# Kernel optimization log

Hardware: AMD Instinct MI355X
Metric: run time of the kernel (lower is better)

## Reference

```python
import jax, jax.numpy as jnp
import numpy as np

B, CIN, COUT, H, W = 8, 64, 64, 32, 64


def _conv3x3(x, w, b):
    # x: [B,Cin,H,W], w: [Cout,Cin,3,3], b: [Cout]; SAME padding (pad=1)
    y = jax.lax.conv_general_dilated(
        x, w, window_strides=(1, 1), padding=((1, 1), (1, 1)),
        dimension_numbers=('NCHW', 'OIHW', 'NCHW'))
    return y + b[None, :, None, None]


def setup_inputs() -> dict:
    key = jax.random.key(0)
    ks = jax.random.split(key, 7)
    fan_in = CIN * 3 * 3
    s = 1.0 / np.sqrt(fan_in)
    x = jax.random.normal(ks[0], (B, CIN, H, W), dtype=jnp.float32)
    wq = jax.random.uniform(ks[1], (COUT, CIN, 3, 3), jnp.float32, -s, s)
    bq = jax.random.uniform(ks[2], (COUT,), jnp.float32, -s, s)
    wk = jax.random.uniform(ks[3], (COUT, CIN, 3, 3), jnp.float32, -s, s)
    bk = jax.random.uniform(ks[4], (COUT,), jnp.float32, -s, s)
    wv = jax.random.uniform(ks[5], (COUT, CIN, 3, 3), jnp.float32, -s, s)
    bv = jax.random.uniform(ks[6], (COUT,), jnp.float32, -s, s)
    return {"x": x, "wq": wq, "bq": bq, "wk": wk, "bk": bk, "wv": wv, "bv": bv}


def reference(x, wq, bq, wk, bk, wv, bv):
    b, _, h, w = x.shape
    n = h * w
    q = _conv3x3(x, wq, bq).reshape(b, COUT, n)  # [B,C,N]
    k = _conv3x3(x, wk, bk).reshape(b, COUT, n)
    v = _conv3x3(x, wv, bv).reshape(b, COUT, n)
    # scores[b, i, j] = sum_c q[b,c,i] * k[b,c,j]  (NOTE: no 1/sqrt(d) scaling, as in source)
    scores = jnp.einsum('bci,bcj->bij', q, k)      # [B,N,N]
    attn = jax.nn.softmax(scores, axis=-1)
    out = jnp.einsum('bij,bcj->bci', attn, v)      # attn @ V^T, then transpose -> [B,C,N]
    return out.reshape(b, COUT, h, w)
```

## Files before the change

kernel.cpp:

```cpp
#include <hip/hip_runtime.h>
#include <hip/hip_bf16.h>

#define BATCH 8
#define NC    64
#define HH    32
#define WW    64
#define NN    2048
#define NCP   72
#define NCHUNK 4

typedef __attribute__((ext_vector_type(8))) short bf16x8;
typedef __attribute__((ext_vector_type(4))) short short4v;
typedef __attribute__((ext_vector_type(4))) float f32x4;

__device__ __forceinline__ unsigned short f2bf(float f) {
    union { float f; unsigned u; } v; v.f = f;
    unsigned r = v.u + 0x7fffu + ((v.u >> 16) & 1u);
    return (unsigned short)(r >> 16);
}
__device__ __forceinline__ float bf2f(unsigned short h) {
    union { unsigned u; float f; } v; v.u = ((unsigned)h) << 16;
    return v.f;
}

__device__ __forceinline__ bf16x8 load8(const unsigned short* a, const unsigned short* b) {
    short4v lo = *(const short4v*)a;
    short4v hi = *(const short4v*)b;
    return __builtin_shufflevector(lo, hi, 0, 1, 2, 3, 4, 5, 6, 7);
}

__device__ __forceinline__ int ci_of_slot(int j) {
    return (j & 32) | (((j >> 2) & 1) << 4) | (((j >> 3) & 3) << 2) | (j & 3);
}

__global__ __launch_bounds__(256) void prep_w(
    const float* __restrict__ wq, const float* __restrict__ wk,
    const float* __restrict__ wv, unsigned short* __restrict__ wb)
{
    const int idx = blockIdx.x * 256 + threadIdx.x;
    if (idx >= 9 * 192 * 64) return;
    const int j    = idx & 63;
    const int row  = (idx >> 6) % 192;
    const int tap  = idx / (192 * 64);
    const int ci   = ci_of_slot(j);
    const int conv = row >> 6;
    const int cout = row & 63;
    const float* ww = (conv == 0) ? wq : (conv == 1) ? wk : wv;
    wb[idx] = f2bf(ww[((size_t)cout * 64 + ci) * 9 + tap]);
}

__global__ __launch_bounds__(256) void prep_x(
    const float* __restrict__ x, unsigned short* __restrict__ xb)
{
    __shared__ unsigned short T[64][72];
    const int bi  = blockIdx.x >> 5;
    const int y   = blockIdx.x & 31;
    const int tid = threadIdx.x;

#pragma unroll
    for (int pass = 0; pass < 16; ++pass) {
        const int idx = pass * 256 + tid;
        const int ci = idx >> 6, xx = idx & 63;
        T[xx][ci] = f2bf(x[(((size_t)bi * 64 + ci) * 32 + y) * 64 + xx]);
    }
    __syncthreads();

#pragma unroll
    for (int pass = 0; pass < 2; ++pass) {
        const int chunk = pass * 256 + tid;
        const int xx = chunk >> 3, j8 = chunk & 7;
        unsigned short h[8];
#pragma unroll
        for (int e = 0; e < 8; ++e)
            h[e] = T[xx][ci_of_slot(j8 * 8 + e)];
        uint4 u;
        u.x = (unsigned)h[0] | ((unsigned)h[1] << 16);
        u.y = (unsigned)h[2] | ((unsigned)h[3] << 16);
        u.z = (unsigned)h[4] | ((unsigned)h[5] << 16);
        u.w = (unsigned)h[6] | ((unsigned)h[7] << 16);
        *(uint4*)(xb + ((((size_t)bi * 32 + y) * 64 + xx) * 64) + j8 * 8) = u;
    }
}

__global__ __launch_bounds__(256) void conv_mfma(
    const unsigned short* __restrict__ xb,
    const unsigned short* __restrict__ wb,
    const float* __restrict__ bq, const float* __restrict__ bk,
    const float* __restrict__ bv,
    unsigned short* __restrict__ qT,
    unsigned short* __restrict__ kT,
    unsigned short* __restrict__ vv)
{
    __shared__ __align__(16) unsigned short Xs[3][66][NCP];
    __shared__ __align__(16) unsigned short Ws[2][96][NCP];

    const int bid = blockIdx.x;
    const int bi  = bid >> 6;
    const int rem = bid & 63;
    const int y   = rem >> 1;
    const int h   = rem & 1;
    const int tid = threadIdx.x;
    const int l   = tid & 63;
    const int w   = tid >> 6;
    const int g   = l >> 4;
    const int li  = l & 15;
    const int mq  = w & 1;
    const int pp  = w >> 1;

#pragma unroll
    for (int r = 0; r < 3; ++r) {
        const int yy = y + r - 1;
#pragma unroll
        for (int pass = 0; pass < 3; ++pass) {
            const int chunk = pass * 256 + tid;
            if (chunk >= 528) break;
            const int c = chunk >> 3, ci8 = chunk & 7;
            uint4 d = {0, 0, 0, 0};
            const int xx = c - 1;
            if (yy >= 0 && yy < HH && xx >= 0 && xx < WW)
                d = *(const uint4*)(xb + ((((size_t)bi * HH + yy) * WW + xx) * 64) + ci8 * 8);
            *(uint4*)&Xs[r][c][ci8 * 8] = d;
        }
    }
#pragma unroll
    for (int pass = 0; pass < 3; ++pass) {
        const int chunk = pass * 256 + tid;
        const int row = chunk >> 3, ci8 = chunk & 7;
        uint4 d = *(const uint4*)(wb + ((size_t)(h * 96 + row)) * 64 + ci8 * 8);
        *(uint4*)&Ws[0][row][ci8 * 8] = d;
    }
    __syncthreads();

    f32x4 acc[2][3];
#pragma unroll
    for (int p2 = 0; p2 < 2; ++p2)
#pragma unroll
        for (int ct = 0; ct < 3; ++ct) acc[p2][ct] = (f32x4){0, 0, 0, 0};

#pragma unroll
    for (int tap = 0; tap < 9; ++tap) {
        const int ky = tap / 3, kx = tap % 3;
        const int cur = tap & 1;

        uint4 wd[3];
        if (tap < 8) {
#pragma unroll
            for (int pass = 0; pass < 3; ++pass) {
                const int chunk = pass * 256 + tid;
                const int row = chunk >> 3, ci8 = chunk & 7;
                wd[pass] = *(const uint4*)(wb + ((size_t)(tap + 1) * 192 + h * 96 + row) * 64 + ci8 * 8);
            }
        }

        bf16x8 xf[2][2];
#pragma unroll
        for (int p2 = 0; p2 < 2; ++p2) {
            const int c = pp * 32 + p2 * 16 + li + kx;
            xf[p2][0] = *(const bf16x8*)&Xs[ky][c][g * 8];
            xf[p2][1] = *(const bf16x8*)&Xs[ky][c][32 + g * 8];
        }

#pragma unroll
        for (int ct = 0; ct < 3; ++ct) {
            const int row = mq * 48 + ct * 16 + li;
            const bf16x8 wf0 = *(const bf16x8*)&Ws[cur][row][g * 8];
            const bf16x8 wf1 = *(const bf16x8*)&Ws[cur][row][32 + g * 8];
            acc[0][ct] = __builtin_amdgcn_mfma_f32_16x16x32_bf16(wf0, xf[0][0], acc[0][ct], 0, 0, 0);
            acc[0][ct] = __builtin_amdgcn_mfma_f32_16x16x32_bf16(wf1, xf[0][1], acc[0][ct], 0, 0, 0);
            acc[1][ct] = __builtin_amdgcn_mfma_f32_16x16x32_bf16(wf0, xf[1][0], acc[1][ct], 0, 0, 0);
            acc[1][ct] = __builtin_amdgcn_mfma_f32_16x16x32_bf16(wf1, xf[1][1], acc[1][ct], 0, 0, 0);
        }

        if (tap < 8) {
#pragma unroll
            for (int pass = 0; pass < 3; ++pass) {
                const int chunk = pass * 256 + tid;
                const int row = chunk >> 3, ci8 = chunk & 7;
                *(uint4*)&Ws[cur ^ 1][row][ci8 * 8] = wd[pass];
            }
            __syncthreads();
        }
    }

#pragma unroll
    for (int p2 = 0; p2 < 2; ++p2) {
        const int n = y * 64 + pp * 32 + p2 * 16 + li;
#pragma unroll
        for (int ct = 0; ct < 3; ++ct) {
            const int rowbase = h * 96 + mq * 48 + ct * 16 + 4 * g;
            const int conv  = rowbase >> 6;
            const int cout0 = rowbase & 63;
            const float* bias = (conv == 0) ? bq : (conv == 1) ? bk : bv;
            float v0 = acc[p2][ct][0] + bias[cout0 + 0];
            float v1 = acc[p2][ct][1] + bias[cout0 + 1];
            float v2 = acc[p2][ct][2] + bias[cout0 + 2];
            float v3 = acc[p2][ct][3] + bias[cout0 + 3];
            if (conv < 2) {
                uint2 pk;
                pk.x = (unsigned)f2bf(v0) | ((unsigned)f2bf(v1) << 16);
                pk.y = (unsigned)f2bf(v2) | ((unsigned)f2bf(v3) << 16);
                unsigned short* dst = ((conv == 0) ? qT : kT) +
                                      ((size_t)bi * NN + n) * NC + cout0;
                *(uint2*)dst = pk;
            } else {
                vv[((size_t)bi * NC + cout0 + 0) * NN + n] = f2bf(v0);
                vv[((size_t)bi * NC + cout0 + 1) * NN + n] = f2bf(v1);
                vv[((size_t)bi * NC + cout0 + 2) * NN + n] = f2bf(v2);
                vv[((size_t)bi * NC + cout0 + 3) * NN + n] = f2bf(v3);
            }
        }
    }
}

__global__ __launch_bounds__(256) void attn_mfma_split(
    const unsigned short* __restrict__ qT,
    const unsigned short* __restrict__ kT,
    const unsigned short* __restrict__ vv,
    unsigned short* __restrict__ Po,
    float* __restrict__ Pm, float* __restrict__ Pl)
{
    __shared__ __align__(16) unsigned short Ks[2][32][72];
    __shared__ __align__(16) unsigned short Vs[2][64][40];

    const int bid  = blockIdx.x;
    const int g8   = bid & 7;
    const int s    = bid >> 3;
    const int qq   = s >> 5;
    const int it   = s & 31;
    const int G    = g8 + 8 * qq;
    const int bi   = G >> 2;
    const int chunk= G & 3;

    const int tid = threadIdx.x;
    const int l   = tid & 63;
    const int w   = tid >> 6;
    const int g   = l >> 4;
    const int li  = l & 15;
    const int i0  = it * 64;
    const int jbase = chunk * (NN / NCHUNK);
    const int NT  = (NN / NCHUNK) / 32;

    const unsigned short* qb = qT + (size_t)bi * NN * NC;
    const unsigned short* kb = kT + (size_t)bi * NN * NC;
    const unsigned short* vb = vv + (size_t)bi * NC * NN;

    const int qrow = i0 + w * 16 + li;
    const bf16x8 qf0 = load8(qb + (size_t)qrow * NC + 4 * g,      qb + (size_t)qrow * NC + 16 + 4 * g);
    const bf16x8 qf1 = load8(qb + (size_t)qrow * NC + 32 + 4 * g, qb + (size_t)qrow * NC + 48 + 4 * g);

    uint4 kd, vd;
    kd = *(const uint4*)(kb + ((size_t)(jbase + (tid >> 3))) * NC + (tid & 7) * 8);
    vd = *(const uint4*)(vb + (size_t)(tid >> 2) * NN + jbase + (tid & 3) * 8);
    *(uint4*)&Ks[0][tid >> 3][(tid & 7) * 8] = kd;
    *(uint4*)&Vs[0][tid >> 2][(tid & 3) * 8] = vd;
    __syncthreads();

    f32x4 o0 = {0,0,0,0}, o1 = {0,0,0,0}, o2 = {0,0,0,0}, o3 = {0,0,0,0};
    float m = -1e30f, lsum = 0.0f;

    for (int t = 0; t < NT; ++t) {
        const int cur = t & 1;
        if (t < NT - 1) {
            const int j0 = jbase + (t + 1) * 32;
            kd = *(const uint4*)(kb + ((size_t)(j0 + (tid >> 3))) * NC + (tid & 7) * 8);
            vd = *(const uint4*)(vb + (size_t)(tid >> 2) * NN + j0 + (tid & 3) * 8);
        }

        const bf16x8 kf00 = load8(&Ks[cur][li][4 * g],           &Ks[cur][li][16 + 4 * g]);
        const bf16x8 kf01 = load8(&Ks[cur][li][32 + 4 * g],      &Ks[cur][li][48 + 4 * g]);
        const bf16x8 kf10 = load8(&Ks[cur][16 + li][4 * g],      &Ks[cur][16 + li][16 + 4 * g]);
        const bf16x8 kf11 = load8(&Ks[cur][16 + li][32 + 4 * g], &Ks[cur][16 + li][48 + 4 * g]);

        const f32x4 z = {0,0,0,0};
        __builtin_amdgcn_s_setprio(1);
        f32x4 d0 = __builtin_amdgcn_mfma_f32_16x16x32_bf16(kf00, qf0, z, 0, 0, 0);
        d0       = __builtin_amdgcn_mfma_f32_16x16x32_bf16(kf01, qf1, d0, 0, 0, 0);
        f32x4 d1 = __builtin_amdgcn_mfma_f32_16x16x32_bf16(kf10, qf0, z, 0, 0, 0);
        d1       = __builtin_amdgcn_mfma_f32_16x16x32_bf16(kf11, qf1, d1, 0, 0, 0);
        __builtin_amdgcn_s_setprio(0);

        float pmax = fmaxf(fmaxf(fmaxf(d0[0], d0[1]), fmaxf(d0[2], d0[3])),
                           fmaxf(fmaxf(d1[0], d1[1]), fmaxf(d1[2], d1[3])));
        pmax = fmaxf(pmax, __shfl_xor(pmax, 16));
        pmax = fmaxf(pmax, __shfl_xor(pmax, 32));

        if (!__all(pmax <= m)) {
            const float mn = fmaxf(m, pmax);
            const float alpha = __expf(m - mn);
            m = mn;
#pragma unroll
            for (int r = 0; r < 4; ++r) {
                const float ar = __shfl(alpha, 4 * g + r, 16);
                o0[r] *= ar; o1[r] *= ar; o2[r] *= ar; o3[r] *= ar;
            }
            lsum *= alpha;
        }

        float p[8];
#pragma unroll
        for (int e = 0; e < 4; ++e) {
            p[e]     = __expf(d0[e] - m);
            p[4 + e] = __expf(d1[e] - m);
        }
        float ls = ((p[0] + p[1]) + (p[2] + p[3])) + ((p[4] + p[5]) + (p[6] + p[7]));
        ls += __shfl_xor(ls, 16);
        ls += __shfl_xor(ls, 32);
        lsum += ls;

        bf16x8 pf;
#pragma unroll
        for (int e = 0; e < 8; ++e) pf[e] = (short)f2bf(p[e]);

        __builtin_amdgcn_s_setprio(1);
        {
            const bf16x8 vf0 = load8(&Vs[cur][li][4 * g],      &Vs[cur][li][16 + 4 * g]);
            o0 = __builtin_amdgcn_mfma_f32_16x16x32_bf16(pf, vf0, o0, 0, 0, 0);
            const bf16x8 vf1 = load8(&Vs[cur][16 + li][4 * g], &Vs[cur][16 + li][16 + 4 * g]);
            o1 = __builtin_amdgcn_mfma_f32_16x16x32_bf16(pf, vf1, o1, 0, 0, 0);
            const bf16x8 vf2 = load8(&Vs[cur][32 + li][4 * g], &Vs[cur][32 + li][16 + 4 * g]);
            o2 = __builtin_amdgcn_mfma_f32_16x16x32_bf16(pf, vf2, o2, 0, 0, 0);
            const bf16x8 vf3 = load8(&Vs[cur][48 + li][4 * g], &Vs[cur][48 + li][16 + 4 * g]);
            o3 = __builtin_amdgcn_mfma_f32_16x16x32_bf16(pf, vf3, o3, 0, 0, 0);
        }
        __builtin_amdgcn_s_setprio(0);

        if (t < NT - 1) {
            *(uint4*)&Ks[cur ^ 1][tid >> 3][(tid & 7) * 8] = kd;
            *(uint4*)&Vs[cur ^ 1][tid >> 2][(tid & 3) * 8] = vd;
        }
        __syncthreads();
    }

    unsigned short* pob = Po + (((size_t)chunk * BATCH + bi) * NN) * NC;
#pragma unroll
    for (int r = 0; r < 4; ++r) {
        const int row = i0 + w * 16 + 4 * g + r;
        unsigned short* pr = pob + (size_t)row * NC;
        pr[0 * 16 + li] = f2bf(o0[r]);
        pr[1 * 16 + li] = f2bf(o1[r]);
        pr[2 * 16 + li] = f2bf(o2[r]);
        pr[3 * 16 + li] = f2bf(o3[r]);
    }
    if (g == 0) {
        const size_t mi = ((size_t)chunk * BATCH + bi) * NN + i0 + w * 16 + li;
        Pm[mi] = m;
        Pl[mi] = lsum;
    }
}

__global__ __launch_bounds__(256) void attn_combine(
    const unsigned short* __restrict__ Po,
    const float* __restrict__ Pm, const float* __restrict__ Pl,
    float* __restrict__ out)
{
    __shared__ float wf[NCHUNK][64];
    __shared__ float Os[64][66];

    const int bi = blockIdx.x >> 5;
    const int it = blockIdx.x & 31;
    const int i0 = it * 64;
    const int tid = threadIdx.x;

    {
        const int ch = tid >> 6, i = tid & 63;
        wf[ch][i] = Pm[((size_t)ch * BATCH + bi) * NN + i0 + i];
    }
    __syncthreads();
    if (tid < 64) {
        float m0 = wf[0][tid], m1 = wf[1][tid], m2 = wf[2][tid], m3 = wf[3][tid];
        const float ms = fmaxf(fmaxf(m0, m1), fmaxf(m2, m3));
        const float e0 = __expf(m0 - ms), e1 = __expf(m1 - ms),
                    e2 = __expf(m2 - ms), e3 = __expf(m3 - ms);
        const float l0 = Pl[((size_t)0 * BATCH + bi) * NN + i0 + tid];
        const float l1 = Pl[((size_t)1 * BATCH + bi) * NN + i0 + tid];
        const float l2 = Pl[((size_t)2 * BATCH + bi) * NN + i0 + tid];
        const float l3 = Pl[((size_t)3 * BATCH + bi) * NN + i0 + tid];
        const float inv = 1.0f / (e0 * l0 + e1 * l1 + e2 * l2 + e3 * l3);
        wf[0][tid] = e0 * inv; wf[1][tid] = e1 * inv;
        wf[2][tid] = e2 * inv; wf[3][tid] = e3 * inv;
    }
    __syncthreads();

    {
        const int rg = tid >> 6, c = tid & 63;
#pragma unroll
        for (int k = 0; k < 16; ++k) {
            const int i = rg * 16 + k;
            float acc = 0.0f;
#pragma unroll
            for (int ch = 0; ch < NCHUNK; ++ch) {
                const float pv = bf2f(Po[(((size_t)ch * BATCH + bi) * NN + i0 + i) * NC + c]);
                acc = fmaf(wf[ch][i], pv, acc);
            }
            Os[i][c] = acc;
        }
    }
    __syncthreads();

    {
        const int c = tid & 63, rg = tid >> 6;
        float* ob = out + ((size_t)bi * NC + c) * NN + i0 + rg * 16;
        float tmp[16];
#pragma unroll
        for (int k = 0; k < 16; ++k) tmp[k] = Os[rg * 16 + k][c];
#pragma unroll
        for (int k = 0; k < 16; k += 4)
            *(float4*)(ob + k) = make_float4(tmp[k], tmp[k+1], tmp[k+2], tmp[k+3]);
    }
}

extern "C" void kernel_launch(void* const* d_in, const int* in_sizes, int n_in,
                              void* d_out, int out_size, void* d_ws, size_t ws_size,
                              hipStream_t stream)
{
    const float* x  = (const float*)d_in[0];
    const float* wq = (const float*)d_in[1];
    const float* bq = (const float*)d_in[2];
    const float* wk = (const float*)d_in[3];
    const float* bk = (const float*)d_in[4];
    const float* wv = (const float*)d_in[5];
    const float* bv = (const float*)d_in[6];

    unsigned short* ws16 = (unsigned short*)d_ws;
    const size_t TEN = (size_t)BATCH * NN * NC;
    unsigned short* qT = ws16;
    unsigned short* kT = ws16 + TEN;
    unsigned short* vv = ws16 + 2 * TEN;
    unsigned short* xb = ws16 + 3 * TEN;
    unsigned short* wb = ws16 + 4 * TEN;
    unsigned short* Po = ws16 + 4 * TEN + 131072;
    float* Pm = (float*)(ws16 + 4 * TEN + 131072 + NCHUNK * TEN);
    float* Pl = Pm + (size_t)NCHUNK * BATCH * NN;
    float* out = (float*)d_out;

    prep_w<<<dim3(432), 256, 0, stream>>>(wq, wk, wv, wb);
    prep_x<<<dim3(256), 256, 0, stream>>>(x, xb);
    conv_mfma<<<dim3(512), 256, 0, stream>>>(xb, wb, bq, bk, bv, qT, kT, vv);
    attn_mfma_split<<<dim3(BATCH * 32 * NCHUNK), 256, 0, stream>>>(qT, kT, vv, Po, Pm, Pl);
    attn_combine<<<dim3(BATCH * 32), 256, 0, stream>>>(Po, Pm, Pl, out);
}
```

Baseline: 60.95 us.

## Double attention split-K chunks and halve conv tile, reading weights from global

```diff
diff --git a/kernel.cpp b/kernel.cpp
--- a/kernel.cpp
+++ b/kernel.cpp
@@ -7,7 +7,7 @@
 #define WW    64
 #define NN    2048
 #define NCP   72
-#define NCHUNK 4
+#define NCHUNK 8
 
 typedef __attribute__((ext_vector_type(8))) short bf16x8;
 typedef __attribute__((ext_vector_type(4))) short short4v;
@@ -91,13 +91,13 @@
     unsigned short* __restrict__ kT,
     unsigned short* __restrict__ vv)
 {
-    __shared__ __align__(16) unsigned short Xs[3][66][NCP];
-    __shared__ __align__(16) unsigned short Ws[2][96][NCP];
+    __shared__ __align__(16) unsigned short Xs[3][34][NCP];
 
     const int bid = blockIdx.x;
-    const int bi  = bid >> 6;
-    const int rem = bid & 63;
-    const int y   = rem >> 1;
+    const int bi  = bid >> 7;
+    const int rem = bid & 127;
+    const int y   = rem >> 2;
+    const int xh  = (rem >> 1) & 1;
     const int h   = rem & 1;
     const int tid = threadIdx.x;
     const int l   = tid & 63;
@@ -106,108 +106,77 @@
     const int li  = l & 15;
     const int mq  = w & 1;
     const int pp  = w >> 1;
-
-#pragma unroll
-    for (int r = 0; r < 3; ++r) {
-        const int yy = y + r - 1;
-#pragma unroll
-        for (int pass = 0; pass < 3; ++pass) {
-            const int chunk = pass * 256 + tid;
-            if (chunk >= 528) break;
-            const int c = chunk >> 3, ci8 = chunk & 7;
+    const int x0  = xh * 32;
+
+#pragma unroll
+    for (int pass = 0; pass < 4; ++pass) {
+        const int chunk = pass * 256 + tid;
+        if (chunk < 816) {
+            const int r  = chunk / 272;
+            const int cc = chunk % 272;
+            const int c  = cc >> 3, ci8 = cc & 7;
+            const int yy = y + r - 1;
+            const int xx = x0 + c - 1;
             uint4 d = {0, 0, 0, 0};
-            const int xx = c - 1;
             if (yy >= 0 && yy < HH && xx >= 0 && xx < WW)
                 d = *(const uint4*)(xb + ((((size_t)bi * HH + yy) * WW + xx) * 64) + ci8 * 8);
             *(uint4*)&Xs[r][c][ci8 * 8] = d;
         }
     }
-#pragma unroll
-    for (int pass = 0; pass < 3; ++pass) {
-        const int chunk = pass * 256 + tid;
-        const int row = chunk >> 3, ci8 = chunk & 7;
-        uint4 d = *(const uint4*)(wb + ((size_t)(h * 96 + row)) * 64 + ci8 * 8);
-        *(uint4*)&Ws[0][row][ci8 * 8] = d;
-    }
-    __syncthreads();
-
-    f32x4 acc[2][3];
-#pragma unroll
-    for (int p2 = 0; p2 < 2; ++p2)
-#pragma unroll
-        for (int ct = 0; ct < 3; ++ct) acc[p2][ct] = (f32x4){0, 0, 0, 0};
+    __syncthreads();
+
+    f32x4 acc[3];
+#pragma unroll
+    for (int ct = 0; ct < 3; ++ct) acc[ct] = (f32x4){0, 0, 0, 0};
+
+    const unsigned short* wrow = wb + ((size_t)(h * 96 + mq * 48 + li)) * 64 + g * 8;
 
 #pragma unroll
     for (int tap = 0; tap < 9; ++tap) {
         const int ky = tap / 3, kx = tap % 3;
-        const int cur = tap & 1;
-
-        uint4 wd[3];
-        if (tap < 8) {
-#pragma unroll
-            for (int pass = 0; pass < 3; ++pass) {
-                const int chunk = pass * 256 + tid;
-                const int row = chunk >> 3, ci8 = chunk & 7;
-                wd[pass] = *(const uint4*)(wb + ((size_t)(tap + 1) * 192 + h * 96 + row) * 64 + ci8 * 8);
-            }
-        }
-
-        bf16x8 xf[2][2];
-#pragma unroll
-        for (int p2 = 0; p2 < 2; ++p2) {
-            const int c = pp * 32 + p2 * 16 + li + kx;
-            xf[p2][0] = *(const bf16x8*)&Xs[ky][c][g * 8];
-            xf[p2][1] = *(const bf16x8*)&Xs[ky][c][32 + g * 8];
-        }
-
+        const unsigned short* wt = wrow + (size_t)tap * (192 * 64);
+
+        bf16x8 wf0[3], wf1[3];
 #pragma unroll
         for (int ct = 0; ct < 3; ++ct) {
-            const int row = mq * 48 + ct * 16 + li;
-            const bf16x8 wf0 = *(const bf16x8*)&Ws[cur][row][g * 8];
-            const bf16x8 wf1 = *(const bf16x8*)&Ws[cur][row][32 + g * 8];
-            acc[0][ct] = __builtin_amdgcn_mfma_f32_16x16x32_bf16(wf0, xf[0][0], acc[0][ct], 0, 0, 0);
-            acc[0][ct] = __builtin_amdgcn_mfma_f32_16x16x32_bf16(wf1, xf[0][1], acc[0][ct], 0, 0, 0);
-            acc[1][ct] = __builtin_amdgcn_mfma_f32_16x16x32_bf16(wf0, xf[1][0], acc[1][ct], 0, 0, 0);
-            acc[1][ct] = __builtin_amdgcn_mfma_f32_16x16x32_bf16(wf1, xf[1][1], acc[1][ct], 0, 0, 0);
-        }
-
-        if (tap < 8) {
-#pragma unroll
-            for (int pass = 0; pass < 3; ++pass) {
-                const int chunk = pass * 256 + tid;
-                const int row = chunk >> 3, ci8 = chunk & 7;
-                *(uint4*)&Ws[cur ^ 1][row][ci8 * 8] = wd[pass];
-            }
-            __syncthreads();
-        }
-    }
-
-#pragma unroll
-    for (int p2 = 0; p2 < 2; ++p2) {
-        const int n = y * 64 + pp * 32 + p2 * 16 + li;
+            wf0[ct] = *(const bf16x8*)(wt + ct * 1024);
+            wf1[ct] = *(const bf16x8*)(wt + ct * 1024 + 32);
+        }
+
+        const int c = pp * 16 + li + kx;
+        const bf16x8 xf0 = *(const bf16x8*)&Xs[ky][c][g * 8];
+        const bf16x8 xf1 = *(const bf16x8*)&Xs[ky][c][32 + g * 8];
+
 #pragma unroll
         for (int ct = 0; ct < 3; ++ct) {
-            const int rowbase = h * 96 + mq * 48 + ct * 16 + 4 * g;
-            const int conv  = rowbase >> 6;
-            const int cout0 = rowbase & 63;
-            const float* bias = (conv == 0) ? bq : (conv == 1) ? bk : bv;
-            float v0 = acc[p2][ct][0] + bias[cout0 + 0];
-            float v1 = acc[p2][ct][1] + bias[cout0 + 1];
-            float v2 = acc[p2][ct][2] + bias[cout0 + 2];
-            float v3 = acc[p2][ct][3] + bias[cout0 + 3];
-            if (conv < 2) {
-                uint2 pk;
-                pk.x = (unsigned)f2bf(v0) | ((unsigned)f2bf(v1) << 16);
-                pk.y = (unsigned)f2bf(v2) | ((unsigned)f2bf(v3) << 16);
-                unsigned short* dst = ((conv == 0) ? qT : kT) +
-                                      ((size_t)bi * NN + n) * NC + cout0;
-                *(uint2*)dst = pk;
-            } else {
-                vv[((size_t)bi * NC + cout0 + 0) * NN + n] = f2bf(v0);
-                vv[((size_t)bi * NC + cout0 + 1) * NN + n] = f2bf(v1);
-                vv[((size_t)bi * NC + cout0 + 2) * NN + n] = f2bf(v2);
-                vv[((size_t)bi * NC + cout0 + 3) * NN + n] = f2bf(v3);
-            }
+            acc[ct] = __builtin_amdgcn_mfma_f32_16x16x32_bf16(wf0[ct], xf0, acc[ct], 0, 0, 0);
+            acc[ct] = __builtin_amdgcn_mfma_f32_16x16x32_bf16(wf1[ct], xf1, acc[ct], 0, 0, 0);
+        }
+    }
+
+    const int n = y * 64 + x0 + pp * 16 + li;
+#pragma unroll
+    for (int ct = 0; ct < 3; ++ct) {
+        const int rowbase = h * 96 + mq * 48 + ct * 16 + 4 * g;
+        const int conv  = rowbase >> 6;
+        const int cout0 = rowbase & 63;
+        const float* bias = (conv == 0) ? bq : (conv == 1) ? bk : bv;
+        float v0 = acc[ct][0] + bias[cout0 + 0];
+        float v1 = acc[ct][1] + bias[cout0 + 1];
+        float v2 = acc[ct][2] + bias[cout0 + 2];
+        float v3 = acc[ct][3] + bias[cout0 + 3];
+        if (conv < 2) {
+            uint2 pk;
+            pk.x = (unsigned)f2bf(v0) | ((unsigned)f2bf(v1) << 16);
+            pk.y = (unsigned)f2bf(v2) | ((unsigned)f2bf(v3) << 16);
+            unsigned short* dst = ((conv == 0) ? qT : kT) +
+                                  ((size_t)bi * NN + n) * NC + cout0;
+            *(uint2*)dst = pk;
+        } else {
+            vv[((size_t)bi * NC + cout0 + 0) * NN + n] = f2bf(v0);
+            vv[((size_t)bi * NC + cout0 + 1) * NN + n] = f2bf(v1);
+            vv[((size_t)bi * NC + cout0 + 2) * NN + n] = f2bf(v2);
+            vv[((size_t)bi * NC + cout0 + 3) * NN + n] = f2bf(v3);
         }
     }
 }
@@ -228,8 +197,8 @@
     const int qq   = s >> 5;
     const int it   = s & 31;
     const int G    = g8 + 8 * qq;
-    const int bi   = G >> 2;
-    const int chunk= G & 3;
+    const int bi   = G >> 3;
+    const int chunk= G & 7;
 
     const int tid = threadIdx.x;
     const int l   = tid & 63;
@@ -361,23 +330,32 @@
     const int i0 = it * 64;
     const int tid = threadIdx.x;
 
-    {
-        const int ch = tid >> 6, i = tid & 63;
+#pragma unroll
+    for (int pass = 0; pass < NCHUNK / 4; ++pass) {
+        const int t = pass * 256 + tid;
+        const int ch = t >> 6, i = t & 63;
         wf[ch][i] = Pm[((size_t)ch * BATCH + bi) * NN + i0 + i];
     }
     __syncthreads();
     if (tid < 64) {
-        float m0 = wf[0][tid], m1 = wf[1][tid], m2 = wf[2][tid], m3 = wf[3][tid];
-        const float ms = fmaxf(fmaxf(m0, m1), fmaxf(m2, m3));
-        const float e0 = __expf(m0 - ms), e1 = __expf(m1 - ms),
-                    e2 = __expf(m2 - ms), e3 = __expf(m3 - ms);
-        const float l0 = Pl[((size_t)0 * BATCH + bi) * NN + i0 + tid];
-        const float l1 = Pl[((size_t)1 * BATCH + bi) * NN + i0 + tid];
-        const float l2 = Pl[((size_t)2 * BATCH + bi) * NN + i0 + tid];
-        const float l3 = Pl[((size_t)3 * BATCH + bi) * NN + i0 + tid];
-        const float inv = 1.0f / (e0 * l0 + e1 * l1 + e2 * l2 + e3 * l3);
-        wf[0][tid] = e0 * inv; wf[1][tid] = e1 * inv;
-        wf[2][tid] = e2 * inv; wf[3][tid] = e3 * inv;
+        float mv[NCHUNK];
+        float ms = -1e30f;
+#pragma unroll
+        for (int ch = 0; ch < NCHUNK; ++ch) {
+            mv[ch] = wf[ch][tid];
+            ms = fmaxf(ms, mv[ch]);
+        }
+        float denom = 0.0f;
+        float ev[NCHUNK];
+#pragma unroll
+        for (int ch = 0; ch < NCHUNK; ++ch) {
+            ev[ch] = __expf(mv[ch] - ms);
+            denom = fmaf(ev[ch], Pl[((size_t)ch * BATCH + bi) * NN + i0 + tid], denom);
+        }
+        const float inv = 1.0f / denom;
+#pragma unroll
+        for (int ch = 0; ch < NCHUNK; ++ch)
+            wf[ch][tid] = ev[ch] * inv;
     }
     __syncthreads();
 
@@ -429,13 +407,13 @@
     unsigned short* xb = ws16 + 3 * TEN;
     unsigned short* wb = ws16 + 4 * TEN;
     unsigned short* Po = ws16 + 4 * TEN + 131072;
-    float* Pm = (float*)(ws16 + 4 * TEN + 131072 + NCHUNK * TEN);
+    float* Pm = (float*)(ws16 + 4 * TEN + 131072 + (size_t)NCHUNK * TEN);
     float* Pl = Pm + (size_t)NCHUNK * BATCH * NN;
     float* out = (float*)d_out;
 
     prep_w<<<dim3(432), 256, 0, stream>>>(wq, wk, wv, wb);
     prep_x<<<dim3(256), 256, 0, stream>>>(x, xb);
-    conv_mfma<<<dim3(512), 256, 0, stream>>>(xb, wb, bq, bk, bv, qT, kT, vv);
+    conv_mfma<<<dim3(1024), 256, 0, stream>>>(xb, wb, bq, bk, bv, qT, kT, vv);
     attn_mfma_split<<<dim3(BATCH * 32 * NCHUNK), 256, 0, stream>>>(qT, kT, vv, Po, Pm, Pl);
     attn_combine<<<dim3(BATCH * 32), 256, 0, stream>>>(Po, Pm, Pl, out);
 }
```

Measured after the change: 77.60 us. 27.3% more time.
